# Performance work log

Hardware: AMD Instinct MI355X
Metric: run time of the kernel (lower is better)

## Reference

```python
import jax, jax.numpy as jnp
import numpy as np


def setup_inputs() -> dict:
    key = jax.random.key(0)
    k1, k2 = jax.random.split(key)
    S_src, S_tgt, B, H = 2048, 2048, 16, 256
    out_e = jax.random.normal(k1, (S_src, B, 2 * H), dtype=jnp.float32)
    out_d = jax.random.normal(k2, (S_tgt, B, H), dtype=jnp.float32)
    return {"out_e": out_e, "out_d": out_d}


def reference(out_e, out_d):
    # out_e: [S_src, B, 2*H] (bidirectional), out_d: [S_tgt, B, H]
    S, B, H2 = out_e.shape
    # sum the two directions: [S, B, H]
    enc = out_e.reshape(S, B, 2, H2 // 2).sum(axis=2)
    enc = enc.transpose(1, 0, 2)   # [B, S_src, H]
    dec = out_d.transpose(1, 0, 2)  # [B, S_tgt, H]
    # attn scores [B, S_src, S_tgt]; softmax over source positions (dim=1)
    attn = jnp.einsum('bsh,bth->bst', enc, dec)
    attn = jax.nn.softmax(attn, axis=1)
    # context: weighted sum over source positions -> [B, S_tgt, H]
    context = jnp.einsum('bst,bsh->bth', attn, enc)
    return context.transpose(1, 0, 2)  # [S_tgt, B, H]
```

## Files before the change

kernel.cpp:

```cpp
#include <hip/hip_runtime.h>
#include <stdint.h>
#include <stddef.h>

#define BATCH 16
#define SEQ 2048
#define HDIM 256
#define SCHUNK 32
#define TTILE 128
#define NCHUNK 64
#define TILE_U16 8192
#define NTILES 1024
#define PREBLK 2048
#define KSTRIDE 260
#define PSTRIDE 40

typedef float f32x4 __attribute__((ext_vector_type(4)));
typedef float f32x16 __attribute__((ext_vector_type(16)));
typedef _Float16 f16x8 __attribute__((ext_vector_type(8)));
typedef __bf16 bf16x8 __attribute__((ext_vector_type(8)));
typedef unsigned short u16;
typedef u16 u16x4 __attribute__((ext_vector_type(4)));
typedef u16 u16x8 __attribute__((ext_vector_type(8)));
typedef unsigned int u32;
typedef u32 u32x2 __attribute__((ext_vector_type(2)));
typedef const __attribute__((address_space(1))) u32* gp1_t;
typedef __attribute__((address_space(3))) u32* lp3_t;

static __device__ __forceinline__ u16 f2bf(float f) {
  union { float f; unsigned int u; } v; v.f = f;
  unsigned int u = v.u;
  unsigned int r = u + 0x7FFFu + ((u >> 16) & 1u);
  return (u16)(r >> 16);
}

__global__ __launch_bounds__(256, 8)
void prepass_kernel(const float* __restrict__ e,
                    u16* __restrict__ KH, u16* __restrict__ VT) {
  __shared__ float Ks[16 * KSTRIDE];
  const int tid = threadIdx.x;
  const int bid = blockIdx.x;
  const int h2  = bid & 1;
  const int tb  = bid >> 1;
  const int b   = tb >> 6;
  const int ck  = tb & 63;
  const size_t tile = (size_t)tb * TILE_U16;
  const int r0 = h2 * 16;

  {
    int row = tid >> 4;
    int c16 = tid & 15;
    const float* src = e + ((size_t)(ck * SCHUNK + r0 + row) * BATCH + b) * (2 * HDIM);
#pragma unroll
    for (int u = 0; u < 4; ++u) {
      int col = c16 * 4 + 64 * u;
      float4 xa = *(const float4*)(src + col);
      float4 xb = *(const float4*)(src + col + HDIM);
      float4 s; s.x = xa.x + xb.x; s.y = xa.y + xb.y; s.z = xa.z + xb.z; s.w = xa.w + xb.w;
      *(float4*)&Ks[row * KSTRIDE + col] = s;
    }
  }
  __syncthreads();

  const int lane = tid & 63;
  const int w = tid >> 6;

  {
    int half = lane >> 5;
    int l5   = lane & 31;
    int lm   = l5 & 15;
    int g    = (l5 >> 4) & 1;
#pragma unroll
    for (int i = 0; i < 2; ++i) {
      int kb = w * 4 + i * 2 + half;
      const float* rp = &Ks[lm * KSTRIDE + kb * 16 + g * 8];
      u16x8 hi;
#pragma unroll
      for (int j = 0; j < 8; ++j)
        hi[j] = __builtin_bit_cast(u16, (_Float16)rp[j]);
      int lane_out = g * 32 + r0 + lm;
      *(u16x8*)&KH[tile + (size_t)(kb * 64 + lane_out) * 8] = hi;
    }
  }

  {
    int m = lane & 31;
    int g = lane >> 5;
#pragma unroll
    for (int i = 0; i < 2; ++i) {
      int ht = w * 2 + i;
      int fr = ht * 2 + h2;
      u16x8 v;
#pragma unroll
      for (int j = 0; j < 8; ++j)
        v[j] = f2bf(Ks[(g * 8 + j) * KSTRIDE + ht * 32 + m]);
      *(u16x8*)&VT[tile + (size_t)(fr * 64 + lane) * 8] = v;
    }
  }
}

__global__ __launch_bounds__(512, 2)
void attn_main_kernel(const u16* __restrict__ KH, const u16* __restrict__ VT,
                      const float* __restrict__ dq,
                      float* __restrict__ out) {
  __shared__ alignas(16) u16 KHs[4][TILE_U16];
  __shared__ alignas(16) u16 VTs[4][TILE_U16];
  __shared__ alignas(16) u16 Pb[8][32 * PSTRIDE];

  const int tid  = threadIdx.x;
  const int lane = tid & 63;
  const int wv   = tid >> 6;
  const int wq   = wv & 3;
  const int grp  = wv >> 2;
  const int m    = lane & 31;
  const int g    = lane >> 5;

  const int bid = blockIdx.x;
  const int b  = ((bid & 7) << 1) | ((bid >> 3) & 1);
  const int t0 = (bid >> 4) * TTILE;

  const int tq = t0 + wq * 32 + m;
  const float* qp = dq + ((size_t)tq * BATCH + b) * HDIM;
  f16x8 qh[16];
#pragma unroll
  for (int kb = 0; kb < 16; ++kb) {
    int h = kb * 16 + g * 8;
    float4 f0 = *(const float4*)(qp + h);
    float4 f1 = *(const float4*)(qp + h + 4);
    float xs[8] = {f0.x, f0.y, f0.z, f0.w, f1.x, f1.y, f1.z, f1.w};
    u16x8 hb;
#pragma unroll
    for (int j = 0; j < 8; ++j)
      hb[j] = __builtin_bit_cast(u16, (_Float16)xs[j]);
    qh[kb] = __builtin_bit_cast(f16x8, hb);
  }

  f32x16 ctx[8];
#pragma unroll
  for (int ht = 0; ht < 8; ++ht) ctx[ht] = (f32x16)(0.0f);
  float dsum = 0.0f;

  const bool isVT  = (wv >> 1) & 1;
  const int  choff = wv >> 2;
  const int  subbase = (wv & 1) * 8;
  const u16* srcArr = isVT ? VT : KH;
  auto stage = [&](int jpair) {
    int ckk = 2 * jpair + choff;
    int buf = ckk & 3;
    size_t tb = ((size_t)b * NCHUNK + ckk) * TILE_U16;
    u16* dst = isVT ? &VTs[buf][0] : &KHs[buf][0];
#pragma unroll
    for (int i = 0; i < 8; ++i) {
      int sub = subbase + i;
      __builtin_amdgcn_global_load_lds(
          (gp1_t)(const void*)&srcArr[tb + (size_t)sub * 512 + lane * 8],
          (lp3_t)(void*)&dst[sub * 512], 16, 0, 0);
    }
  };

  stage(0);

  for (int j = 0; j < 32; ++j) {
    if (j < 31) {
      stage(j + 1);
      asm volatile("s_waitcnt vmcnt(8)" ::: "memory");
    } else {
      asm volatile("s_waitcnt vmcnt(0)" ::: "memory");
    }
    __builtin_amdgcn_s_barrier();
    __builtin_amdgcn_sched_barrier(0);

    const int ckk = 2 * j + grp;
    const int buf = ckk & 3;

    f32x16 a0 = (f32x16)(0.0f), a1 = (f32x16)(0.0f);
    __builtin_amdgcn_s_setprio(1);
#pragma unroll
    for (int kb = 0; kb < 16; kb += 2) {
      f16x8 k0 = __builtin_bit_cast(f16x8, *(const u16x8*)&KHs[buf][kb * 512 + lane * 8]);
      f16x8 k1 = __builtin_bit_cast(f16x8, *(const u16x8*)&KHs[buf][(kb + 1) * 512 + lane * 8]);
      a0 = __builtin_amdgcn_mfma_f32_32x32x16_f16(k0, qh[kb], a0, 0, 0, 0);
      a1 = __builtin_amdgcn_mfma_f32_32x32x16_f16(k1, qh[kb + 1], a1, 0, 0, 0);
    }
    __builtin_amdgcn_s_setprio(0);

    float pf[16];
#pragma unroll
    for (int r = 0; r < 16; ++r) {
      pf[r] = __expf(a0[r] + a1[r] - 128.0f);
      dsum += pf[r];
    }
    u32 pk[8];
#pragma unroll
    for (int q = 0; q < 8; ++q)
      asm("v_cvt_pk_bf16_f32 %0, %1, %2"
          : "=v"(pk[q]) : "v"(pf[2 * q]), "v"(pf[2 * q + 1]));
#pragma unroll
    for (int rr = 0; rr < 4; ++rr) {
      u32x2 w2 = {pk[2 * rr], pk[2 * rr + 1]};
      *(u32x2*)&Pb[wv][m * PSTRIDE + rr * 8 + g * 4] = w2;
    }
    bf16x8 pa0 = __builtin_bit_cast(bf16x8, *(const u16x8*)&Pb[wv][m * PSTRIDE + g * 8]);
    bf16x8 pa1 = __builtin_bit_cast(bf16x8, *(const u16x8*)&Pb[wv][m * PSTRIDE + 16 + g * 8]);

    __builtin_amdgcn_s_setprio(1);
#pragma unroll
    for (int ht = 0; ht < 8; ++ht) {
      bf16x8 v0 = __builtin_bit_cast(bf16x8, *(const u16x8*)&VTs[buf][(ht * 2) * 512 + lane * 8]);
      bf16x8 v1 = __builtin_bit_cast(bf16x8, *(const u16x8*)&VTs[buf][(ht * 2 + 1) * 512 + lane * 8]);
      ctx[ht] = __builtin_amdgcn_mfma_f32_32x32x16_bf16(pa0, v0, ctx[ht], 0, 0, 0);
      ctx[ht] = __builtin_amdgcn_mfma_f32_32x32x16_bf16(pa1, v1, ctx[ht], 0, 0, 0);
    }
    __builtin_amdgcn_s_setprio(0);

    __builtin_amdgcn_sched_barrier(0);
    __builtin_amdgcn_s_barrier();
  }

  dsum += __shfl_xor(dsum, 32, 64);
  __syncthreads();

  float* exch = (wq < 2) ? (float*)&KHs[wq * 2][0] : (float*)&VTs[(wq - 2) * 2][0];

  if (grp == 1) {
#pragma unroll
    for (int r4 = 0; r4 < 4; ++r4)
#pragma unroll
      for (int ht = 0; ht < 8; ++ht) {
        f32x4 v = {ctx[ht][r4 * 4], ctx[ht][r4 * 4 + 1],
                   ctx[ht][r4 * 4 + 2], ctx[ht][r4 * 4 + 3]};
        *(f32x4*)&exch[r4 * 2048 + ht * 256 + lane * 4] = v;
      }
    ((float*)&Pb[wv][0])[lane] = dsum;
  }
  __syncthreads();

  if (grp == 0) {
    float dB = ((const float*)&Pb[wv + 4][0])[lane];
    float inv = 1.0f / (dsum + dB);
#pragma unroll
    for (int r4 = 0; r4 < 4; ++r4)
#pragma unroll
      for (int ht = 0; ht < 8; ++ht) {
        f32x4 v = *(const f32x4*)&exch[r4 * 2048 + ht * 256 + lane * 4];
        ctx[ht][r4 * 4]     += v[0];
        ctx[ht][r4 * 4 + 1] += v[1];
        ctx[ht][r4 * 4 + 2] += v[2];
        ctx[ht][r4 * 4 + 3] += v[3];
      }
#pragma unroll
    for (int r = 0; r < 16; ++r) {
      int tl = (r & 3) + 8 * (r >> 2) + 4 * g;
      float rinv = __shfl(inv, tl, 64);
      int t = t0 + wq * 32 + tl;
      float* op = out + ((size_t)t * BATCH + b) * HDIM + m;
#pragma unroll
      for (int ht = 0; ht < 8; ++ht)
        op[ht * 32] = ctx[ht][r] * rinv;
    }
  }
}

extern "C" void kernel_launch(void* const* d_in, const int* in_sizes, int n_in,
                              void* d_out, int out_size, void* d_ws, size_t ws_size,
                              hipStream_t stream) {
  const float* e  = (const float*)d_in[0];
  const float* dq = (const float*)d_in[1];
  float* out = (float*)d_out;
  u16* KH = (u16*)d_ws;
  u16* VT = KH + (size_t)NTILES * TILE_U16;
  prepass_kernel<<<dim3(PREBLK), dim3(256), 0, stream>>>(e, KH, VT);
  attn_main_kernel<<<dim3(BATCH * (SEQ / TTILE)), dim3(512), 0, stream>>>(
      KH, VT, dq, out);
}
```

Measured before the change: 204.2 us.

## Software-pipeline QK of next chunk with PV and pass P via permlane swap

```diff
diff --git a/kernel.cpp b/kernel.cpp
--- a/kernel.cpp
+++ b/kernel.cpp
@@ -12,17 +12,15 @@
 #define NTILES 1024
 #define PREBLK 2048
 #define KSTRIDE 260
-#define PSTRIDE 40
 
 typedef float f32x4 __attribute__((ext_vector_type(4)));
 typedef float f32x16 __attribute__((ext_vector_type(16)));
 typedef _Float16 f16x8 __attribute__((ext_vector_type(8)));
 typedef __bf16 bf16x8 __attribute__((ext_vector_type(8)));
 typedef unsigned short u16;
-typedef u16 u16x4 __attribute__((ext_vector_type(4)));
 typedef u16 u16x8 __attribute__((ext_vector_type(8)));
 typedef unsigned int u32;
-typedef u32 u32x2 __attribute__((ext_vector_type(2)));
+typedef u32 u32x4 __attribute__((ext_vector_type(4)));
 typedef const __attribute__((address_space(1))) u32* gp1_t;
 typedef __attribute__((address_space(3))) u32* lp3_t;
 
@@ -103,8 +101,7 @@
                       const float* __restrict__ dq,
                       float* __restrict__ out) {
   __shared__ alignas(16) u16 KHs[4][TILE_U16];
-  __shared__ alignas(16) u16 VTs[4][TILE_U16];
-  __shared__ alignas(16) u16 Pb[8][32 * PSTRIDE];
+  __shared__ alignas(16) u16 VTs[6][TILE_U16];
 
   const int tid  = threadIdx.x;
   const int lane = tid & 63;
@@ -138,16 +135,18 @@
 #pragma unroll
   for (int ht = 0; ht < 8; ++ht) ctx[ht] = (f32x16)(0.0f);
   float dsum = 0.0f;
+  bf16x8 pa0 = {}, pa1 = {};
 
   const bool isVT  = (wv >> 1) & 1;
   const int  choff = wv >> 2;
   const int  subbase = (wv & 1) * 8;
   const u16* srcArr = isVT ? VT : KH;
-  auto stage = [&](int jpair) {
-    int ckk = 2 * jpair + choff;
-    int buf = ckk & 3;
+  auto stage = [&](int p) {
+    int ckk = 2 * p + choff;
+    int ktile = 2 * (p & 1) + choff;
+    int vtile = (p % 3) * 2 + choff;
     size_t tb = ((size_t)b * NCHUNK + ckk) * TILE_U16;
-    u16* dst = isVT ? &VTs[buf][0] : &KHs[buf][0];
+    u16* dst = isVT ? &VTs[vtile][0] : &KHs[ktile][0];
 #pragma unroll
     for (int i = 0; i < 8; ++i) {
       int sub = subbase + i;
@@ -157,69 +156,81 @@
     }
   };
 
-  stage(0);
-
-  for (int j = 0; j < 32; ++j) {
-    if (j < 31) {
-      stage(j + 1);
-      asm volatile("s_waitcnt vmcnt(8)" ::: "memory");
-    } else {
-      asm volatile("s_waitcnt vmcnt(0)" ::: "memory");
-    }
-    __builtin_amdgcn_s_barrier();
-    __builtin_amdgcn_sched_barrier(0);
-
-    const int ckk = 2 * j + grp;
-    const int buf = ckk & 3;
-
-    f32x16 a0 = (f32x16)(0.0f), a1 = (f32x16)(0.0f);
-    __builtin_amdgcn_s_setprio(1);
+  auto qk = [&](int p, f32x16& a0, f32x16& a1) {
+    int kt = 2 * (p & 1) + grp;
 #pragma unroll
     for (int kb = 0; kb < 16; kb += 2) {
-      f16x8 k0 = __builtin_bit_cast(f16x8, *(const u16x8*)&KHs[buf][kb * 512 + lane * 8]);
-      f16x8 k1 = __builtin_bit_cast(f16x8, *(const u16x8*)&KHs[buf][(kb + 1) * 512 + lane * 8]);
+      f16x8 k0 = __builtin_bit_cast(f16x8, *(const u16x8*)&KHs[kt][kb * 512 + lane * 8]);
+      f16x8 k1 = __builtin_bit_cast(f16x8, *(const u16x8*)&KHs[kt][(kb + 1) * 512 + lane * 8]);
       a0 = __builtin_amdgcn_mfma_f32_32x32x16_f16(k0, qh[kb], a0, 0, 0, 0);
       a1 = __builtin_amdgcn_mfma_f32_32x32x16_f16(k1, qh[kb + 1], a1, 0, 0, 0);
     }
-    __builtin_amdgcn_s_setprio(0);
-
+  };
+
+  auto pv = [&](int p) {
+    int vt_ = (p % 3) * 2 + grp;
+#pragma unroll
+    for (int ht = 0; ht < 8; ++ht) {
+      bf16x8 v0 = __builtin_bit_cast(bf16x8, *(const u16x8*)&VTs[vt_][(ht * 2) * 512 + lane * 8]);
+      bf16x8 v1 = __builtin_bit_cast(bf16x8, *(const u16x8*)&VTs[vt_][(ht * 2 + 1) * 512 + lane * 8]);
+      ctx[ht] = __builtin_amdgcn_mfma_f32_32x32x16_bf16(pa0, v0, ctx[ht], 0, 0, 0);
+      ctx[ht] = __builtin_amdgcn_mfma_f32_32x32x16_bf16(pa1, v1, ctx[ht], 0, 0, 0);
+    }
+  };
+
+  auto softmax_pack = [&](const f32x16& a0, const f32x16& a1) {
     float pf[16];
 #pragma unroll
     for (int r = 0; r < 16; ++r) {
       pf[r] = __expf(a0[r] + a1[r] - 128.0f);
       dsum += pf[r];
     }
-    u32 pk[8];
+    u32 c[8];
 #pragma unroll
     for (int q = 0; q < 8; ++q)
       asm("v_cvt_pk_bf16_f32 %0, %1, %2"
-          : "=v"(pk[q]) : "v"(pf[2 * q]), "v"(pf[2 * q + 1]));
-#pragma unroll
-    for (int rr = 0; rr < 4; ++rr) {
-      u32x2 w2 = {pk[2 * rr], pk[2 * rr + 1]};
-      *(u32x2*)&Pb[wv][m * PSTRIDE + rr * 8 + g * 4] = w2;
-    }
-    bf16x8 pa0 = __builtin_bit_cast(bf16x8, *(const u16x8*)&Pb[wv][m * PSTRIDE + g * 8]);
-    bf16x8 pa1 = __builtin_bit_cast(bf16x8, *(const u16x8*)&Pb[wv][m * PSTRIDE + 16 + g * 8]);
-
+          : "=v"(c[q]) : "v"(pf[2 * q]), "v"(pf[2 * q + 1]));
+    asm("v_permlane32_swap_b32 %0, %1" : "+v"(c[0]), "+v"(c[2]));
+    asm("v_permlane32_swap_b32 %0, %1" : "+v"(c[1]), "+v"(c[3]));
+    asm("v_permlane32_swap_b32 %0, %1" : "+v"(c[4]), "+v"(c[6]));
+    asm("v_permlane32_swap_b32 %0, %1" : "+v"(c[5]), "+v"(c[7]));
+    u32x4 w0 = {c[0], c[1], c[2], c[3]};
+    u32x4 w1 = {c[4], c[5], c[6], c[7]};
+    pa0 = __builtin_bit_cast(bf16x8, w0);
+    pa1 = __builtin_bit_cast(bf16x8, w1);
+  };
+
+  stage(0);
+  stage(1);
+  asm volatile("s_waitcnt vmcnt(8)" ::: "memory");
+  __builtin_amdgcn_s_barrier();
+  {
+    f32x16 a0 = (f32x16)(0.0f), a1 = (f32x16)(0.0f);
+    qk(0, a0, a1);
+    softmax_pack(a0, a1);
+  }
+
+  for (int j = 0; j < 32; ++j) {
+    asm volatile("s_waitcnt vmcnt(0)" ::: "memory");
+    __builtin_amdgcn_s_barrier();
+    if (j < 30) stage(j + 2);
+
+    f32x16 a0 = (f32x16)(0.0f), a1 = (f32x16)(0.0f);
     __builtin_amdgcn_s_setprio(1);
-#pragma unroll
-    for (int ht = 0; ht < 8; ++ht) {
-      bf16x8 v0 = __builtin_bit_cast(bf16x8, *(const u16x8*)&VTs[buf][(ht * 2) * 512 + lane * 8]);
-      bf16x8 v1 = __builtin_bit_cast(bf16x8, *(const u16x8*)&VTs[buf][(ht * 2 + 1) * 512 + lane * 8]);
-      ctx[ht] = __builtin_amdgcn_mfma_f32_32x32x16_bf16(pa0, v0, ctx[ht], 0, 0, 0);
-      ctx[ht] = __builtin_amdgcn_mfma_f32_32x32x16_bf16(pa1, v1, ctx[ht], 0, 0, 0);
-    }
+    if (j < 31) qk(j + 1, a0, a1);
+    pv(j);
     __builtin_amdgcn_s_setprio(0);
-
-    __builtin_amdgcn_sched_barrier(0);
-    __builtin_amdgcn_s_barrier();
+    if (j < 31) softmax_pack(a0, a1);
   }
 
   dsum += __shfl_xor(dsum, 32, 64);
   __syncthreads();
 
-  float* exch = (wq < 2) ? (float*)&KHs[wq * 2][0] : (float*)&VTs[(wq - 2) * 2][0];
+  float* exch = (wq == 0) ? (float*)&KHs[0][0]
+              : (wq == 1) ? (float*)&KHs[2][0]
+              : (wq == 2) ? (float*)&VTs[0][0]
+                          : (float*)&VTs[2][0];
+  float* dex = (float*)&VTs[4][0];
 
   if (grp == 1) {
 #pragma unroll
@@ -230,12 +241,12 @@
                    ctx[ht][r4 * 4 + 2], ctx[ht][r4 * 4 + 3]};
         *(f32x4*)&exch[r4 * 2048 + ht * 256 + lane * 4] = v;
       }
-    ((float*)&Pb[wv][0])[lane] = dsum;
+    dex[wq * 64 + lane] = dsum;
   }
   __syncthreads();
 
   if (grp == 0) {
-    float dB = ((const float*)&Pb[wv + 4][0])[lane];
+    float dB = dex[wq * 64 + lane];
     float inv = 1.0f / (dsum + dB);
 #pragma unroll
     for (int r4 = 0; r4 < 4; ++r4)
```

After: 200.8 us. No clear change (-1.7%).
